# Optimization experiments

Hardware: AMD Instinct MI355X
Metric: run time of the kernel (lower is better)

The kernel has to match this reference:

```python
import jax, jax.numpy as jnp
import numpy as np

KAPPA = 0.5  # decorrelation loss mixing coefficient (init kwarg)


def setup_inputs() -> dict:
    key = jax.random.key(0)
    kx, kw, kb, kd, ki = jax.random.split(key, 5)
    b, l, d = 4, 8192, 1024
    n_samples = int(0.25 * l)  # sample_frac = 0.25
    x = jax.random.normal(kx, (b, l, d), dtype=jnp.float32)
    W = jax.random.normal(kw, (d, d), dtype=jnp.float32) * 0.02
    bias = jax.random.normal(kb, (d,), dtype=jnp.float32) * 0.02
    # decorr_layer is initialized at identity in the module; perturb slightly so the
    # decorrelation matmul is non-trivial (it gets updated during training).
    decorr = jnp.eye(d, dtype=jnp.float32) + 0.01 * jax.random.normal(kd, (d, d), dtype=jnp.float32)
    sample_idx = jax.random.randint(ki, (b, n_samples), 0, l)  # stand-in for torch.multinomial
    return {"x": x, "W": W, "bias": bias, "decorr": decorr, "sample_idx": sample_idx}


def reference(x, W, bias, decorr, sample_idx):
    # Output path: y = x @ (W @ decorr)^T + bias
    y = jnp.einsum('bld,od->blo', x, W @ decorr) + bias

    b, l, d = x.shape
    # Gather sampled tokens: [b, n, d]
    selected = jnp.take_along_axis(x, sample_idx[:, :, None], axis=1)
    xs = (selected @ decorr.T).reshape(-1, d)  # [N, d], N = b*n_samples
    N = xs.shape[0]

    # DecorrLoss, algebraically reduced (same math as diag_embed/outer-product form):
    #   C_n = x_n x_n^T - diag(x_n^2)  (zero diagonal, off-diag x_i x_j)
    #   V_n = diag(x_n^2) - I          (diagonal x_i^2 - 1, zero off-diag)
    X2 = xs * xs                     # [N, d]
    m2 = jnp.mean(X2, axis=0)        # [d], mean of x_i^2
    S = X2.T @ X2                    # [d, d]; S_ij = sum_n x_ni^2 x_nj^2
    denom = jnp.float32(N) * d * d
    correlation_loss = (jnp.sum(S) - jnp.trace(S)) / denom       # mean_n mean_ij C_n^2
    whitening_loss = jnp.sum((X2 - 1.0) ** 2) / denom             # mean_n mean_ij V_n^2

    G = (xs.T @ xs) / N              # mean_n x_n x_n^T
    C_mean = G - jnp.diag(m2)
    V_mean = jnp.diag(m2) - jnp.eye(d, dtype=xs.dtype)
    grad = (1.0 - KAPPA) * C_mean + KAPPA * V_mean

    return y, grad, correlation_loss, whitening_loss
```

## Files before the change

kernel.cpp:

```cpp
#include <hip/hip_runtime.h>
#include <cstdint>
#include <cstddef>

typedef __bf16 bf16x8 __attribute__((ext_vector_type(8)));
typedef float  f32x4  __attribute__((ext_vector_type(4)));
typedef unsigned short u16x4 __attribute__((ext_vector_type(4)));

typedef __attribute__((address_space(1))) void* gas1_t;
typedef __attribute__((address_space(3))) void* las3_t;

__device__ __forceinline__ unsigned short f2bf(float f) {
  union { float f; unsigned u; } v; v.f = f;
  unsigned r = v.u + 0x7fffu + ((v.u >> 16) & 1u);
  return (unsigned short)(r >> 16);
}
__device__ __forceinline__ float bf2f(unsigned short h) {
  union { unsigned u; float f; } v; v.u = ((unsigned)h) << 16;
  return v.f;
}

constexpr int Bc = 4, Lc = 8192, Dc = 1024, NSAMP = 2048;
constexpr int ROWS = Bc * Lc;
constexpr int NSEL = Bc * NSAMP;
constexpr long long Y_ELEMS = (long long)ROWS * Dc;
constexpr long long GRAD_OFF = Y_ELEMS;
constexpr long long LOSS_OFF = GRAD_OFF + (long long)Dc*Dc;

constexpr int BM = 128, BN = 128, BK = 64;

template<int MODE>
__global__ void gemm_bt(const unsigned short* __restrict__ A,
                        const unsigned short* __restrict__ B,
                        float* __restrict__ Cf,
                        const float* __restrict__ bias,
                        int M, int N, int K, int kchunk) {
  __shared__ unsigned short sA[BM * BK];
  __shared__ unsigned short sB[BN * BK];
  const int tid  = threadIdx.x;
  const int lane = tid & 63;
  const int wave = tid >> 6;
  const int wm = wave >> 1, wn = wave & 1;
  const int q = lane >> 4, r16 = lane & 15;

  int m0, n0;
  if constexpr (MODE == 6) {
    int t = blockIdx.x, ti = 0;
    while (t >= 8 - ti) { t -= 8 - ti; ++ti; }
    m0 = ti * BM; n0 = (ti + t) * BN;
  } else {
    const int gx   = gridDim.x;
    const int nwg  = gx * gridDim.y;
    const int orig = blockIdx.y * gx + blockIdx.x;
    const int swz  = (orig & 7) * (nwg >> 3) + (orig >> 3);
    m0 = (swz / gx) * BM;
    n0 = (swz % gx) * BN;
  }
  const int kb = blockIdx.z * kchunk;

  const int lrow = lane >> 3;
  const int lcol = (lane & 7) * 8;

  f32x4 acc[4][4] = {};

  for (int k0 = kb; k0 < kb + kchunk; k0 += BK) {
#pragma unroll
    for (int j = 0; j < 4; ++j) {
      const int c = wave * 4 + j;
      const int row = c * 8 + lrow;
      const unsigned short* ga = A + (size_t)(m0 + row) * K + k0 + lcol;
      __builtin_amdgcn_global_load_lds((gas1_t)(void*)ga, (las3_t)(sA + c * 512), 16, 0, 0);
      const unsigned short* gb = B + (size_t)(n0 + row) * K + k0 + lcol;
      __builtin_amdgcn_global_load_lds((gas1_t)(void*)gb, (las3_t)(sB + c * 512), 16, 0, 0);
    }
    __syncthreads();
#pragma unroll
    for (int kk = 0; kk < BK; kk += 32) {
      bf16x8 af[4], bfv[4];
#pragma unroll
      for (int mi = 0; mi < 4; ++mi)
        af[mi] = *(const bf16x8*)(sA + (size_t)(wm*64 + mi*16 + r16) * BK + kk + q*8);
#pragma unroll
      for (int ni = 0; ni < 4; ++ni)
        bfv[ni] = *(const bf16x8*)(sB + (size_t)(wn*64 + ni*16 + r16) * BK + kk + q*8);
#pragma unroll
      for (int mi = 0; mi < 4; ++mi)
#pragma unroll
        for (int ni = 0; ni < 4; ++ni)
          acc[mi][ni] = __builtin_amdgcn_mfma_f32_16x16x32_bf16(af[mi], bfv[ni], acc[mi][ni], 0, 0, 0);
    }
    __syncthreads();
  }

  const int row0 = m0 + wm*64 + q*4;
  const int col0 = n0 + wn*64 + r16;
  float bv[4] = {0.f, 0.f, 0.f, 0.f};
  if (MODE == 0) {
#pragma unroll
    for (int ni = 0; ni < 4; ++ni) bv[ni] = bias[col0 + ni*16];
  }
#pragma unroll
  for (int mi = 0; mi < 4; ++mi) {
#pragma unroll
    for (int r = 0; r < 4; ++r) {
      const int row = row0 + mi*16 + r;
      const size_t base = (size_t)row * N + col0;
#pragma unroll
      for (int ni = 0; ni < 4; ++ni) {
        const size_t o = base + (size_t)ni * 16;
        float v = acc[mi][ni][r];
        if (MODE == 0)      __builtin_nontemporal_store(v + bv[ni], &Cf[o]);
        else if (MODE == 5) ((unsigned short*)Cf)[o] = f2bf(v);
        else                atomicAdd(&Cf[o], v);
      }
    }
  }
}

__global__ __launch_bounds__(256)
void xs_gemm_fused(const unsigned short* __restrict__ A,
                   const unsigned short* __restrict__ B,
                   const float* __restrict__ cvec,
                   unsigned short* __restrict__ xsT,
                   float* __restrict__ m2sum, float* __restrict__ s1g,
                   float* __restrict__ s2g,
                   int M, int N, int K) {
  __shared__ __attribute__((aligned(16))) unsigned short shm[128 * 136];
  unsigned short* sA = shm;
  unsigned short* sB = shm + 8192;
  const int tid  = threadIdx.x;
  const int lane = tid & 63;
  const int wave = tid >> 6;
  const int wm = wave >> 1, wn = wave & 1;
  const int q = lane >> 4, r16 = lane & 15;

  const int gx   = gridDim.x;
  const int nwg  = gx * gridDim.y;
  const int orig = blockIdx.y * gx + blockIdx.x;
  const int swz  = (orig & 7) * (nwg >> 3) + (orig >> 3);
  const int m0 = (swz / gx) * BM;
  const int n0 = (swz % gx) * BN;

  const int lrow = lane >> 3;
  const int lcol = (lane & 7) * 8;

  f32x4 acc[4][4] = {};

  for (int k0 = 0; k0 < K; k0 += BK) {
#pragma unroll
    for (int j = 0; j < 4; ++j) {
      const int c = wave * 4 + j;
      const int row = c * 8 + lrow;
      const unsigned short* ga = A + (size_t)(m0 + row) * K + k0 + lcol;
      __builtin_amdgcn_global_load_lds((gas1_t)(void*)ga, (las3_t)(sA + c * 512), 16, 0, 0);
      const unsigned short* gb = B + (size_t)(n0 + row) * K + k0 + lcol;
      __builtin_amdgcn_global_load_lds((gas1_t)(void*)gb, (las3_t)(sB + c * 512), 16, 0, 0);
    }
    __syncthreads();
#pragma unroll
    for (int kk = 0; kk < BK; kk += 32) {
      bf16x8 af[4], bfv[4];
#pragma unroll
      for (int mi = 0; mi < 4; ++mi)
        af[mi] = *(const bf16x8*)(sA + (size_t)(wm*64 + mi*16 + r16) * BK + kk + q*8);
#pragma unroll
      for (int ni = 0; ni < 4; ++ni)
        bfv[ni] = *(const bf16x8*)(sB + (size_t)(wn*64 + ni*16 + r16) * BK + kk + q*8);
#pragma unroll
      for (int mi = 0; mi < 4; ++mi)
#pragma unroll
        for (int ni = 0; ni < 4; ++ni)
          acc[mi][ni] = __builtin_amdgcn_mfma_f32_16x16x32_bf16(af[mi], bfv[ni], acc[mi][ni], 0, 0, 0);
    }
    __syncthreads();
  }

  const int lr0 = wm*64 + q*4;
  const int lc0 = wn*64 + r16;
  float cvl[4];
#pragma unroll
  for (int ni = 0; ni < 4; ++ni) cvl[ni] = cvec[n0 + lc0 + ni*16];
#pragma unroll
  for (int mi = 0; mi < 4; ++mi) {
#pragma unroll
    for (int r = 0; r < 4; ++r) {
      const int lr = lr0 + mi*16 + r;
      const size_t arow = (size_t)(m0 + lr) * K;
#pragma unroll
      for (int ni = 0; ni < 4; ++ni) {
        const int lc = lc0 + ni*16;
        float v = acc[mi][ni][r] + bf2f(A[arow + n0 + lc]) * cvl[ni];
        shm[lr * 136 + lc] = f2bf(v);
      }
    }
  }
  __syncthreads();

  if (tid < 128) {
    float s1 = 0.f, s2 = 0.f;
#pragma unroll 8
    for (int c = 0; c < 128; ++c) {
      float v = bf2f(shm[tid * 136 + c]); float v2 = v * v;
      s1 += v2; s2 += v2 * v2;
    }
    atomicAdd(&s1g[m0 + tid], s1);
    atomicAdd(&s2g[m0 + tid], s2);
  } else {
    const int col = tid - 128;
    float cs = 0.f;
#pragma unroll 8
    for (int r = 0; r < 128; ++r) {
      float v = bf2f(shm[r * 136 + col]); cs += v * v;
    }
    atomicAdd(&m2sum[n0 + col], cs);
  }

  const int fi = tid >> 1, hh = tid & 1;
  unsigned short* dst = xsT + (size_t)(n0 + fi) * M + m0 + hh * 64;
#pragma unroll
  for (int j = 0; j < 64; j += 4) {
    u16x4 v;
    v.x = shm[(hh*64 + j + 0) * 136 + fi];
    v.y = shm[(hh*64 + j + 1) * 136 + fi];
    v.z = shm[(hh*64 + j + 2) * 136 + fi];
    v.w = shm[(hh*64 + j + 3) * 136 + fi];
    *(u16x4*)(dst + j) = v;
  }
}

template<int NT>
__global__ void cvt_f32_bf16(const float* __restrict__ in, unsigned short* __restrict__ out, long long n) {
  long long i = ((long long)blockIdx.x * 256 + threadIdx.x) * 4;
  if (i >= n) return;
  f32x4 v;
  if (NT) v = __builtin_nontemporal_load((const f32x4*)(in + i));
  else    v = *(const f32x4*)(in + i);
  u16x4 o;
  o.x = f2bf(v.x); o.y = f2bf(v.y); o.z = f2bf(v.z); o.w = f2bf(v.w);
  *(u16x4*)(out + i) = o;
}

__global__ void gather_rows(const unsigned short* __restrict__ xb, const int* __restrict__ idx,
                            unsigned short* __restrict__ out) {
  const int blk = blockIdx.x;
  const int b = blk >> 11, n = blk & 2047;
  const int row = idx[b * NSAMP + n];
  const unsigned short* src = xb + ((size_t)b * Lc + row) * Dc;
  unsigned short* dst = out + (size_t)blk * Dc;
  const int c = threadIdx.x * 4;
  *(u16x4*)(dst + c) = *(const u16x4*)(src + c);
}

__global__ void prep_wdt(const float* __restrict__ W, const float* __restrict__ dc,
                         unsigned short* __restrict__ wb, unsigned short* __restrict__ dT,
                         float* __restrict__ cvec) {
  __shared__ float tile[64][65];
  const int r0 = blockIdx.y * 64, c0 = blockIdx.x * 64;
  const int t = threadIdx.x;
  const int c = t & 63, r4 = t >> 6;
#pragma unroll
  for (int j = 0; j < 16; ++j) {
    const int r = j * 4 + r4;
    const size_t o = (size_t)(r0 + r) * Dc + c0 + c;
    wb[o] = f2bf(W[o]);
    tile[r][c] = dc[o];
  }
  __syncthreads();
  if (blockIdx.x == blockIdx.y && t < 64) {
    const float v = tile[t][t];
    cvec[c0 + t] = v - bf2f(f2bf(v));
  }
  const int i = t >> 2, p = t & 3;
  unsigned short* dst = dT + (size_t)(c0 + i) * Dc + r0 + p * 16;
#pragma unroll
  for (int j = 0; j < 16; j += 4) {
    u16x4 v;
    v.x = f2bf(tile[p*16 + j + 0][i]);
    v.y = f2bf(tile[p*16 + j + 1][i]);
    v.z = f2bf(tile[p*16 + j + 2][i]);
    v.w = f2bf(tile[p*16 + j + 3][i]);
    *(u16x4*)(dst + j) = v;
  }
}

__global__ void grad_write(const float* __restrict__ G, const float* __restrict__ m2sum,
                           float* __restrict__ out) {
  const int i = blockIdx.x * 256 + threadIdx.x;
  const int r = i >> 10, c = i & 1023;
  int rr = r, cc = c;
  if ((r >> 7) > (c >> 7)) { rr = c; cc = r; }
  float g = G[rr * 1024 + cc] * (0.5f / (float)NSEL);
  if (r == c) g = 0.5f * (m2sum[r] * (1.0f / (float)NSEL) - 1.0f);
  __builtin_nontemporal_store(g, &out[i]);
}

__global__ void finalize_losses(const float* __restrict__ s1g, const float* __restrict__ s2g,
                                float* __restrict__ out2) {
  __shared__ double sa[256], sb[256], sc[256];
  double a = 0, b = 0, c = 0;
  for (int n = threadIdx.x; n < NSEL; n += 256) {
    double s1 = s1g[n], s2 = s2g[n];
    a += s1 * s1; b += s2; c += s1;
  }
  const int t = threadIdx.x;
  sa[t] = a; sb[t] = b; sc[t] = c;
  __syncthreads();
  for (int s = 128; s > 0; s >>= 1) {
    if (t < s) { sa[t] += sa[t+s]; sb[t] += sb[t+s]; sc[t] += sc[t+s]; }
    __syncthreads();
  }
  if (t == 0) {
    const double denom = (double)NSEL * (double)Dc * (double)Dc;
    const double cnt   = (double)NSEL * (double)Dc;
    out2[0] = (float)((sa[0] - sb[0]) / denom);
    out2[1] = (float)((sb[0] - 2.0 * sc[0] + cnt) / denom);
  }
}

extern "C" void kernel_launch(void* const* d_in, const int* in_sizes, int n_in,
                              void* d_out, int out_size, void* d_ws, size_t ws_size,
                              hipStream_t stream) {
  const float* x      = (const float*)d_in[0];
  const float* W      = (const float*)d_in[1];
  const float* bias   = (const float*)d_in[2];
  const float* decorr = (const float*)d_in[3];
  const int*   sidx   = (const int*)d_in[4];
  float* out = (float*)d_out;

  char* w = (char*)d_ws;
  constexpr size_t SZ_XB  = (size_t)ROWS * Dc * 2;
  constexpr size_t SZ_AB  = (size_t)NSEL * Dc * 2;
  constexpr size_t SZ_DT  = (size_t)Dc * Dc * 2;
  constexpr size_t SZ_WB  = (size_t)Dc * Dc * 2;
  constexpr size_t SZ_MB  = (size_t)Dc * Dc * 2;
  constexpr size_t SZ_XST = (size_t)Dc * NSEL * 2;
  constexpr size_t SZ_CV  = (size_t)Dc * 4;
  constexpr size_t SZ_GB  = (size_t)Dc * Dc * 4;
  constexpr size_t SZ_M2  = (size_t)Dc * 4;
  constexpr size_t SZ_S1  = (size_t)NSEL * 4;
  constexpr size_t SZ_S2  = (size_t)NSEL * 4;

  size_t off = 0;
  unsigned short* xb  = (unsigned short*)(w + off); off += SZ_XB;
  unsigned short* ab  = (unsigned short*)(w + off); off += SZ_AB;
  unsigned short* dT  = (unsigned short*)(w + off); off += SZ_DT;
  unsigned short* wb  = (unsigned short*)(w + off); off += SZ_WB;
  unsigned short* mb  = (unsigned short*)(w + off); off += SZ_MB;
  unsigned short* xsT = (unsigned short*)(w + off); off += SZ_XST;
  float*          cv  = (float*)(w + off);          off += SZ_CV;
  char*           zbase = w + off;
  float*          Gb  = (float*)(w + off);          off += SZ_GB;
  float*          m2s = (float*)(w + off);          off += SZ_M2;
  float*          s1g = (float*)(w + off);          off += SZ_S1;
  float*          s2g = (float*)(w + off);          off += SZ_S2;
  const size_t zbytes = SZ_GB + SZ_M2 + SZ_S1 + SZ_S2;

  (void)hipMemsetAsync(zbase, 0, zbytes, stream);

  cvt_f32_bf16<1><<<(int)(Y_ELEMS / 1024), 256, 0, stream>>>(x, xb, Y_ELEMS);
  prep_wdt<<<dim3(16, 16), 256, 0, stream>>>(W, decorr, wb, dT, cv);
  gather_rows<<<NSEL, 256, 0, stream>>>(xb, sidx, ab);

  gemm_bt<5><<<dim3(Dc/BN, Dc/BM, 1), 256, 0, stream>>>(wb, dT, (float*)mb, nullptr, Dc, Dc, Dc, Dc);

  gemm_bt<0><<<dim3(Dc/BN, ROWS/BM, 1), 256, 0, stream>>>(xb, mb, out, bias, ROWS, Dc, Dc, Dc);

  xs_gemm_fused<<<dim3(Dc/BN, NSEL/BM), 256, 0, stream>>>(ab, dT, cv, xsT, m2s, s1g, s2g,
                                                          NSEL, Dc, Dc);

  gemm_bt<6><<<dim3(36, 1, 8), 256, 0, stream>>>(xsT, xsT, Gb, nullptr, Dc, Dc, NSEL, NSEL/8);

  grad_write<<<Dc*Dc / 256, 256, 0, stream>>>(Gb, m2s, out + GRAD_OFF);
  finalize_losses<<<1, 256, 0, stream>>>(s1g, s2g, out + LOSS_OFF);
}
```

Baseline: 422.5 us.

## Fuse fp32-to-bf16 conversion into main GEMM and replace split-K atomics with partials

The standalone pass that converted all of x to bf16 is removed. The y GEMM now loads fp32 x directly, converts it in registers and stores it into LDS, and gather_rows converts the sampled rows itself. The Gram GEMM no longer atomically adds into a triangular grid. It writes per-tile partial sums for all 64 tiles across 8 k-slices, and grad_write reduces them. This avoids writing and re-reading a large bf16 copy of x and avoids atomics and the memset of G, but the y GEMM now reads A synchronously without global_load_lds and the Gram step computes the full square instead of the triangle.

```diff
diff --git a/kernel.cpp b/kernel.cpp
--- a/kernel.cpp
+++ b/kernel.cpp
@@ -28,11 +28,93 @@
 
 constexpr int BM = 128, BN = 128, BK = 64;
 
+__global__ __launch_bounds__(256)
+void gemm_y(const float* __restrict__ A,
+            const unsigned short* __restrict__ B,
+            float* __restrict__ Cf,
+            const float* __restrict__ bias,
+            int M, int N, int K) {
+  __shared__ unsigned short sA[BM * BK];
+  __shared__ unsigned short sB[BN * BK];
+  const int tid  = threadIdx.x;
+  const int lane = tid & 63;
+  const int wave = tid >> 6;
+  const int wm = wave >> 1, wn = wave & 1;
+  const int q = lane >> 4, r16 = lane & 15;
+
+  const int gx   = gridDim.x;
+  const int nwg  = gx * gridDim.y;
+  const int orig = blockIdx.y * gx + blockIdx.x;
+  const int swz  = (orig & 7) * (nwg >> 3) + (orig >> 3);
+  const int m0 = (swz / gx) * BM;
+  const int n0 = (swz % gx) * BN;
+
+  const int lrow = lane >> 3;
+  const int lcol = (lane & 7) * 8;
+  const int arow = tid >> 4;
+  const int acol = (tid & 15) * 4;
+
+  f32x4 acc[4][4] = {};
+
+  for (int k0 = 0; k0 < K; k0 += BK) {
+    f32x4 av[8];
+#pragma unroll
+    for (int it = 0; it < 8; ++it)
+      av[it] = *(const f32x4*)(A + (size_t)(m0 + arow + it * 16) * K + k0 + acol);
+#pragma unroll
+    for (int j = 0; j < 4; ++j) {
+      const int c = wave * 4 + j;
+      const unsigned short* gb = B + (size_t)(n0 + c * 8 + lrow) * K + k0 + lcol;
+      __builtin_amdgcn_global_load_lds((gas1_t)(void*)gb, (las3_t)(sB + c * 512), 16, 0, 0);
+    }
+#pragma unroll
+    for (int it = 0; it < 8; ++it) {
+      u16x4 o;
+      o.x = f2bf(av[it].x); o.y = f2bf(av[it].y);
+      o.z = f2bf(av[it].z); o.w = f2bf(av[it].w);
+      *(u16x4*)(sA + (arow + it * 16) * BK + acol) = o;
+    }
+    __syncthreads();
+#pragma unroll
+    for (int kk = 0; kk < BK; kk += 32) {
+      bf16x8 af[4], bfv[4];
+#pragma unroll
+      for (int mi = 0; mi < 4; ++mi)
+        af[mi] = *(const bf16x8*)(sA + (size_t)(wm*64 + mi*16 + r16) * BK + kk + q*8);
+#pragma unroll
+      for (int ni = 0; ni < 4; ++ni)
+        bfv[ni] = *(const bf16x8*)(sB + (size_t)(wn*64 + ni*16 + r16) * BK + kk + q*8);
+#pragma unroll
+      for (int mi = 0; mi < 4; ++mi)
+#pragma unroll
+        for (int ni = 0; ni < 4; ++ni)
+          acc[mi][ni] = __builtin_amdgcn_mfma_f32_16x16x32_bf16(af[mi], bfv[ni], acc[mi][ni], 0, 0, 0);
+    }
+    __syncthreads();
+  }
+
+  const int row0 = m0 + wm*64 + q*4;
+  const int col0 = n0 + wn*64 + r16;
+  float bv[4];
+#pragma unroll
+  for (int ni = 0; ni < 4; ++ni) bv[ni] = bias[col0 + ni*16];
+#pragma unroll
+  for (int mi = 0; mi < 4; ++mi) {
+#pragma unroll
+    for (int r = 0; r < 4; ++r) {
+      const int row = row0 + mi*16 + r;
+      const size_t base = (size_t)row * N + col0;
+#pragma unroll
+      for (int ni = 0; ni < 4; ++ni)
+        __builtin_nontemporal_store(acc[mi][ni][r] + bv[ni], &Cf[base + (size_t)ni * 16]);
+    }
+  }
+}
+
 template<int MODE>
 __global__ void gemm_bt(const unsigned short* __restrict__ A,
                         const unsigned short* __restrict__ B,
                         float* __restrict__ Cf,
-                        const float* __restrict__ bias,
                         int M, int N, int K, int kchunk) {
   __shared__ unsigned short sA[BM * BK];
   __shared__ unsigned short sB[BN * BK];
@@ -42,19 +124,12 @@
   const int wm = wave >> 1, wn = wave & 1;
   const int q = lane >> 4, r16 = lane & 15;
 
-  int m0, n0;
-  if constexpr (MODE == 6) {
-    int t = blockIdx.x, ti = 0;
-    while (t >= 8 - ti) { t -= 8 - ti; ++ti; }
-    m0 = ti * BM; n0 = (ti + t) * BN;
-  } else {
-    const int gx   = gridDim.x;
-    const int nwg  = gx * gridDim.y;
-    const int orig = blockIdx.y * gx + blockIdx.x;
-    const int swz  = (orig & 7) * (nwg >> 3) + (orig >> 3);
-    m0 = (swz / gx) * BM;
-    n0 = (swz % gx) * BN;
-  }
+  const int gx   = gridDim.x;
+  const int nwg  = gx * gridDim.y;
+  const int orig = blockIdx.y * gx + blockIdx.x;
+  const int swz  = (orig & 7) * (nwg >> 3) + (orig >> 3);
+  const int m0 = (swz / gx) * BM;
+  const int n0 = (swz % gx) * BN;
   const int kb = blockIdx.z * kchunk;
 
   const int lrow = lane >> 3;
@@ -93,24 +168,20 @@
 
   const int row0 = m0 + wm*64 + q*4;
   const int col0 = n0 + wn*64 + r16;
-  float bv[4] = {0.f, 0.f, 0.f, 0.f};
-  if (MODE == 0) {
-#pragma unroll
-    for (int ni = 0; ni < 4; ++ni) bv[ni] = bias[col0 + ni*16];
-  }
+  float* dst7 = nullptr;
+  if (MODE == 7)
+    dst7 = Cf + ((size_t)blockIdx.z * 64 + (size_t)(m0 >> 7) * 8 + (n0 >> 7)) * 16384;
 #pragma unroll
   for (int mi = 0; mi < 4; ++mi) {
 #pragma unroll
     for (int r = 0; r < 4; ++r) {
       const int row = row0 + mi*16 + r;
-      const size_t base = (size_t)row * N + col0;
 #pragma unroll
       for (int ni = 0; ni < 4; ++ni) {
-        const size_t o = base + (size_t)ni * 16;
+        const int col = col0 + ni*16;
         float v = acc[mi][ni][r];
-        if (MODE == 0)      __builtin_nontemporal_store(v + bv[ni], &Cf[o]);
-        else if (MODE == 5) ((unsigned short*)Cf)[o] = f2bf(v);
-        else                atomicAdd(&Cf[o], v);
+        if (MODE == 5)      ((unsigned short*)Cf)[(size_t)row * N + col] = f2bf(v);
+        else                dst7[(size_t)(row - m0) * 128 + (col - n0)] = v;
       }
     }
   }
@@ -227,27 +298,18 @@
   }
 }
 
-template<int NT>
-__global__ void cvt_f32_bf16(const float* __restrict__ in, unsigned short* __restrict__ out, long long n) {
-  long long i = ((long long)blockIdx.x * 256 + threadIdx.x) * 4;
-  if (i >= n) return;
-  f32x4 v;
-  if (NT) v = __builtin_nontemporal_load((const f32x4*)(in + i));
-  else    v = *(const f32x4*)(in + i);
-  u16x4 o;
-  o.x = f2bf(v.x); o.y = f2bf(v.y); o.z = f2bf(v.z); o.w = f2bf(v.w);
-  *(u16x4*)(out + i) = o;
-}
-
-__global__ void gather_rows(const unsigned short* __restrict__ xb, const int* __restrict__ idx,
+__global__ void gather_rows(const float* __restrict__ x, const int* __restrict__ idx,
                             unsigned short* __restrict__ out) {
   const int blk = blockIdx.x;
   const int b = blk >> 11, n = blk & 2047;
   const int row = idx[b * NSAMP + n];
-  const unsigned short* src = xb + ((size_t)b * Lc + row) * Dc;
+  const float* src = x + ((size_t)b * Lc + row) * Dc;
   unsigned short* dst = out + (size_t)blk * Dc;
   const int c = threadIdx.x * 4;
-  *(u16x4*)(dst + c) = *(const u16x4*)(src + c);
+  f32x4 v = *(const f32x4*)(src + c);
+  u16x4 o;
+  o.x = f2bf(v.x); o.y = f2bf(v.y); o.z = f2bf(v.z); o.w = f2bf(v.w);
+  *(u16x4*)(dst + c) = o;
 }
 
 __global__ void prep_wdt(const float* __restrict__ W, const float* __restrict__ dc,
@@ -282,13 +344,16 @@
   }
 }
 
-__global__ void grad_write(const float* __restrict__ G, const float* __restrict__ m2sum,
+__global__ void grad_write(const float* __restrict__ Gp, const float* __restrict__ m2sum,
                            float* __restrict__ out) {
   const int i = blockIdx.x * 256 + threadIdx.x;
   const int r = i >> 10, c = i & 1023;
-  int rr = r, cc = c;
-  if ((r >> 7) > (c >> 7)) { rr = c; cc = r; }
-  float g = G[rr * 1024 + cc] * (0.5f / (float)NSEL);
+  const size_t tidx = (size_t)((r >> 7) * 8 + (c >> 7));
+  const float* base = Gp + tidx * 16384 + (size_t)(r & 127) * 128 + (c & 127);
+  float s = 0.f;
+#pragma unroll
+  for (int z = 0; z < 8; ++z) s += base[(size_t)z * 64 * 16384];
+  float g = s * (0.5f / (float)NSEL);
   if (r == c) g = 0.5f * (m2sum[r] * (1.0f / (float)NSEL) - 1.0f);
   __builtin_nontemporal_store(g, &out[i]);
 }
@@ -327,48 +392,45 @@
   float* out = (float*)d_out;
 
   char* w = (char*)d_ws;
-  constexpr size_t SZ_XB  = (size_t)ROWS * Dc * 2;
   constexpr size_t SZ_AB  = (size_t)NSEL * Dc * 2;
   constexpr size_t SZ_DT  = (size_t)Dc * Dc * 2;
   constexpr size_t SZ_WB  = (size_t)Dc * Dc * 2;
   constexpr size_t SZ_MB  = (size_t)Dc * Dc * 2;
   constexpr size_t SZ_XST = (size_t)Dc * NSEL * 2;
   constexpr size_t SZ_CV  = (size_t)Dc * 4;
-  constexpr size_t SZ_GB  = (size_t)Dc * Dc * 4;
+  constexpr size_t SZ_GP  = (size_t)8 * 64 * 128 * 128 * 4;
   constexpr size_t SZ_M2  = (size_t)Dc * 4;
   constexpr size_t SZ_S1  = (size_t)NSEL * 4;
   constexpr size_t SZ_S2  = (size_t)NSEL * 4;
 
   size_t off = 0;
-  unsigned short* xb  = (unsigned short*)(w + off); off += SZ_XB;
   unsigned short* ab  = (unsigned short*)(w + off); off += SZ_AB;
   unsigned short* dT  = (unsigned short*)(w + off); off += SZ_DT;
   unsigned short* wb  = (unsigned short*)(w + off); off += SZ_WB;
   unsigned short* mb  = (unsigned short*)(w + off); off += SZ_MB;
   unsigned short* xsT = (unsigned short*)(w + off); off += SZ_XST;
   float*          cv  = (float*)(w + off);          off += SZ_CV;
+  float*          Gp  = (float*)(w + off);          off += SZ_GP;
   char*           zbase = w + off;
-  float*          Gb  = (float*)(w + off);          off += SZ_GB;
   float*          m2s = (float*)(w + off);          off += SZ_M2;
   float*          s1g = (float*)(w + off);          off += SZ_S1;
   float*          s2g = (float*)(w + off);          off += SZ_S2;
-  const size_t zbytes = SZ_GB + SZ_M2 + SZ_S1 + SZ_S2;
+  const size_t zbytes = SZ_M2 + SZ_S1 + SZ_S2;
 
   (void)hipMemsetAsync(zbase, 0, zbytes, stream);
 
-  cvt_f32_bf16<1><<<(int)(Y_ELEMS / 1024), 256, 0, stream>>>(x, xb, Y_ELEMS);
   prep_wdt<<<dim3(16, 16), 256, 0, stream>>>(W, decorr, wb, dT, cv);
-  gather_rows<<<NSEL, 256, 0, stream>>>(xb, sidx, ab);
-
-  gemm_bt<5><<<dim3(Dc/BN, Dc/BM, 1), 256, 0, stream>>>(wb, dT, (float*)mb, nullptr, Dc, Dc, Dc, Dc);
-
-  gemm_bt<0><<<dim3(Dc/BN, ROWS/BM, 1), 256, 0, stream>>>(xb, mb, out, bias, ROWS, Dc, Dc, Dc);
+  gather_rows<<<NSEL, 256, 0, stream>>>(x, sidx, ab);
+
+  gemm_bt<5><<<dim3(Dc/BN, Dc/BM, 1), 256, 0, stream>>>(wb, dT, (float*)mb, Dc, Dc, Dc, Dc);
+
+  gemm_y<<<dim3(Dc/BN, ROWS/BM), 256, 0, stream>>>(x, mb, out, bias, ROWS, Dc, Dc);
 
   xs_gemm_fused<<<dim3(Dc/BN, NSEL/BM), 256, 0, stream>>>(ab, dT, cv, xsT, m2s, s1g, s2g,
                                                           NSEL, Dc, Dc);
 
-  gemm_bt<6><<<dim3(36, 1, 8), 256, 0, stream>>>(xsT, xsT, Gb, nullptr, Dc, Dc, NSEL, NSEL/8);
-
-  grad_write<<<Dc*Dc / 256, 256, 0, stream>>>(Gb, m2s, out + GRAD_OFF);
+  gemm_bt<7><<<dim3(Dc/BN, Dc/BM, 8), 256, 0, stream>>>(xsT, xsT, Gp, Dc, Dc, NSEL, NSEL/8);
+
+  grad_write<<<Dc*Dc / 256, 256, 0, stream>>>(Gp, m2s, out + GRAD_OFF);
   finalize_losses<<<1, 256, 0, stream>>>(s1g, s2g, out + LOSS_OFF);
 }
```

New measurement: 465.5 us. +10.2%, slower.
